# Optimization experiments

Measured on AMD Instinct MI355X. Metric: run time of the kernel, lower is better.

The kernel has to match this reference:

```python
import jax, jax.numpy as jnp
import numpy as np

NEG_SLOPE = 0.2
LN_EPS = 1e-5


def setup_inputs() -> dict:
    key = jax.random.key(0)
    ks = jax.random.split(key, 8)
    N, F, d, L, H = 100000, 128, 64, 3, 4
    dh = d // H
    E = 1600000
    return {
        "x": jax.random.normal(ks[0], (N, F), dtype=jnp.float32),
        "edge_index": jax.random.randint(ks[1], (2, E), 0, N, dtype=jnp.int64),
        "W_enc": jax.random.normal(ks[2], (F, d), dtype=jnp.float32) / np.sqrt(F),
        "b_enc": jnp.zeros((d,), jnp.float32),
        "Wl": jax.random.normal(ks[3], (L, d, d), dtype=jnp.float32) / np.sqrt(d),
        "bl": jnp.zeros((L, d), jnp.float32),
        "Wr": jax.random.normal(ks[4], (L, d, d), dtype=jnp.float32) / np.sqrt(d),
        "br": jnp.zeros((L, d), jnp.float32),
        "att": jax.random.normal(ks[5], (L, H, dh), dtype=jnp.float32) / np.sqrt(dh),
        "out_bias": jnp.zeros((L, d), jnp.float32),
        "gamma": jnp.ones((L, d), jnp.float32),
        "beta": jnp.zeros((L, d), jnp.float32),
    }


def _elu(x):
    return jnp.where(x > 0, x, jnp.expm1(x))


def reference(x, edge_index, W_enc, b_enc, Wl, bl, Wr, br, att, out_bias, gamma, beta):
    N = x.shape[0]
    L, H, dh = att.shape
    d = H * dh
    # PyG GATv2Conv default add_self_loops=True
    loops = jnp.arange(N, dtype=edge_index.dtype)
    src = jnp.concatenate([edge_index[0], loops])  # message source
    dst = jnp.concatenate([edge_index[1], loops])  # aggregation target

    h = jax.nn.relu(x @ W_enc + b_enc)  # [N, d]
    for l in range(L):
        xl = (h @ Wl[l] + bl[l]).reshape(N, H, dh)
        xr = (h @ Wr[l] + br[l]).reshape(N, H, dh)
        # GATv2: score = a^T LeakyReLU(xl[src] + xr[dst])  -> [E, H]
        e = jax.nn.leaky_relu(xl[src] + xr[dst], NEG_SLOPE)
        score = jnp.einsum('ehd,hd->eh', e, att[l])
        # segment softmax over incoming edges of each dst node
        smax = jax.ops.segment_max(score, dst, num_segments=N)
        ex = jnp.exp(score - smax[dst])
        denom = jax.ops.segment_sum(ex, dst, num_segments=N)
        alpha = ex / denom[dst]  # [E, H]
        agg = jax.ops.segment_sum(alpha[:, :, None] * xl[src], dst, num_segments=N)
        hc = agg.reshape(N, d) + out_bias[l]
        # LayerNorm
        mu = hc.mean(-1, keepdims=True)
        var = ((hc - mu) ** 2).mean(-1, keepdims=True)
        hn = (hc - mu) * jax.lax.rsqrt(var + LN_EPS) * gamma[l] + beta[l]
        h = _elu(hn)  # dropout p=0.0 -> identity
    return h
```

## Files before the change

### kernel.cpp

```cpp
#include <hip/hip_runtime.h>
#include <hip/hip_fp16.h>
#include <math.h>

static constexpr int D = 64;
static constexpr int F = 128;
static constexpr int BK = 64;
static constexpr float NEG_SLOPE = 0.2f;
static constexpr float LN_EPS = 1e-5f;
static constexpr float LOG2E = 1.44269504088896340736f;
static constexpr int NCHUNK = 8;

template <int CTRL>
__device__ __forceinline__ float dpp_add(float x) {
  int v = __builtin_amdgcn_update_dpp(0, __float_as_int(x), CTRL, 0xF, 0xF, true);
  return x + __int_as_float(v);
}
__device__ __forceinline__ float red8(float x) {
  x = dpp_add<0xB1>(x);
  x = dpp_add<0x4E>(x);
  x = dpp_add<0x141>(x);
  return x;
}
__device__ __forceinline__ float red16(float x) {
  x = red8(x);
  x = dpp_add<0x140>(x);
  return x;
}
__device__ __forceinline__ float red32(float x) {
  x = red16(x);
  x += __shfl_xor(x, 16);
  return x;
}

__device__ __forceinline__ __half2 h2max(__half2 a, __half2 b) {
  int ai = __builtin_bit_cast(int, a), bi = __builtin_bit_cast(int, b), r;
  asm("v_pk_max_f16 %0, %1, %2" : "=v"(r) : "v"(ai), "v"(bi));
  return __builtin_bit_cast(__half2, r);
}

typedef _Float16 half2_t __attribute__((ext_vector_type(2)));
__device__ __forceinline__ float fdot2f(__half2 a, __half2 b) {
#if __has_builtin(__builtin_amdgcn_fdot2)
  return __builtin_amdgcn_fdot2(__builtin_bit_cast(half2_t, a),
                                __builtin_bit_cast(half2_t, b), 0.f, false);
#else
  float2 af = __half22float2(a), bf = __half22float2(b);
  return fmaf(af.x, bf.x, af.y * bf.y);
#endif
}


__global__ __launch_bounds__(256) void k_scatter(const int* __restrict__ src,
                                                 const int* __restrict__ dst,
                                                 int* __restrict__ cursor,
                                                 int* __restrict__ ssrc, int E, int N) {
  int c = blockIdx.x & (NCHUNK - 1);
  int b0 = (c * N) / NCHUNK, b1 = ((c + 1) * N) / NCHUNK;
  int stride = (gridDim.x / NCHUNK) * 256;
  for (int e = (blockIdx.x >> 3) * 256 + threadIdx.x; e < E; e += stride) {
    int d = dst[e];
    if (d >= b0 && d < b1) {
      int p = atomicAdd(&cursor[d], 1);
      if (p < BK) ssrc[(d << 6) + p] = src[e];
    }
  }
}


__global__ __launch_bounds__(256) void k_encoder(const float* __restrict__ x,
                                                 const float* __restrict__ W,
                                                 const float* __restrict__ b,
                                                 float* __restrict__ h, int N) {
  __shared__ float xT[F][64];
  __shared__ float Ws[F][64];
  int t = threadIdx.x;
  int n0 = blockIdx.x * 64;
  for (int i = t; i < F * D / 4; i += 256)
    ((float4*)&Ws[0][0])[i] = ((const float4*)W)[i];
  {
    int r = t & 63, kq = (t >> 6) * 4;
    int n = n0 + r;
#pragma unroll
    for (int i = 0; i < 8; ++i) {
      int k0 = kq + 16 * i;
      float4 v = (n < N) ? *(const float4*)&x[(size_t)n * F + k0]
                         : make_float4(0.f, 0.f, 0.f, 0.f);
      xT[k0][r] = v.x; xT[k0 + 1][r] = v.y; xT[k0 + 2][r] = v.z; xT[k0 + 3][r] = v.w;
    }
  }
  __syncthreads();
  int c4 = (t & 15) * 4, n4 = (t >> 4) * 4;
  float acc[4][4];
#pragma unroll
  for (int i = 0; i < 4; ++i)
#pragma unroll
    for (int j = 0; j < 4; ++j) acc[i][j] = b[c4 + j];
#pragma unroll 4
  for (int k = 0; k < F; ++k) {
    float4 xv = *(const float4*)&xT[k][n4];
    float4 wv = *(const float4*)&Ws[k][c4];
    const float* xp = (const float*)&xv;
    const float* wp = (const float*)&wv;
#pragma unroll
    for (int i = 0; i < 4; ++i)
#pragma unroll
      for (int j = 0; j < 4; ++j) acc[i][j] = fmaf(xp[i], wp[j], acc[i][j]);
  }
#pragma unroll
  for (int i = 0; i < 4; ++i) {
    int n = n0 + n4 + i;
    if (n < N) {
      float4 o = make_float4(fmaxf(acc[i][0], 0.f), fmaxf(acc[i][1], 0.f),
                             fmaxf(acc[i][2], 0.f), fmaxf(acc[i][3], 0.f));
      *(float4*)&h[(size_t)n * D + c4] = o;
    }
  }
}


__global__ __launch_bounds__(256) void k_layer_gemm(const float* __restrict__ h,
                                                    const float* __restrict__ Wl,
                                                    const float* __restrict__ bl,
                                                    const float* __restrict__ Wr,
                                                    const float* __restrict__ br,
                                                    ushort* __restrict__ xlh,
                                                    float* __restrict__ xr, int N) {
  __shared__ float hT[D][64];
  __shared__ float Wls[D][64];
  __shared__ float Wrs[D][64];
  int t = threadIdx.x;
  int n0 = blockIdx.x * 64;
  for (int i = t; i < D * D / 4; i += 256) {
    ((float4*)&Wls[0][0])[i] = ((const float4*)Wl)[i];
    ((float4*)&Wrs[0][0])[i] = ((const float4*)Wr)[i];
  }
  {
    int r = t & 63, kq = (t >> 6) * 4;
    int n = n0 + r;
#pragma unroll
    for (int i = 0; i < 4; ++i) {
      int k0 = kq + 16 * i;
      float4 v = (n < N) ? *(const float4*)&h[(size_t)n * D + k0]
                         : make_float4(0.f, 0.f, 0.f, 0.f);
      hT[k0][r] = v.x; hT[k0 + 1][r] = v.y; hT[k0 + 2][r] = v.z; hT[k0 + 3][r] = v.w;
    }
  }
  __syncthreads();
  int c4 = (t & 15) * 4, n4 = (t >> 4) * 4;
  float aL[4][4], aR[4][4];
#pragma unroll
  for (int i = 0; i < 4; ++i)
#pragma unroll
    for (int j = 0; j < 4; ++j) { aL[i][j] = bl[c4 + j]; aR[i][j] = br[c4 + j]; }
#pragma unroll 4
  for (int k = 0; k < D; ++k) {
    float4 xv = *(const float4*)&hT[k][n4];
    float4 lv = *(const float4*)&Wls[k][c4];
    float4 rv = *(const float4*)&Wrs[k][c4];
    const float* xp = (const float*)&xv;
    const float* lp = (const float*)&lv;
    const float* rp = (const float*)&rv;
#pragma unroll
    for (int i = 0; i < 4; ++i)
#pragma unroll
      for (int j = 0; j < 4; ++j) {
        aL[i][j] = fmaf(xp[i], lp[j], aL[i][j]);
        aR[i][j] = fmaf(xp[i], rp[j], aR[i][j]);
      }
  }
#pragma unroll
  for (int i = 0; i < 4; ++i) {
    int n = n0 + n4 + i;
    if (n < N) {
      ushort4 o;
      o.x = __half_as_ushort(__float2half_rn(aL[i][0]));
      o.y = __half_as_ushort(__float2half_rn(aL[i][1]));
      o.z = __half_as_ushort(__float2half_rn(aL[i][2]));
      o.w = __half_as_ushort(__float2half_rn(aL[i][3]));
      *(ushort4*)&xlh[(size_t)n * D + c4] = o;
      *(float4*)&xr[(size_t)n * D + c4] =
          make_float4(aR[i][0], aR[i][1], aR[i][2], aR[i][3]);
    }
  }
}


template <int P>
__device__ __forceinline__ void batchH(const char* __restrict__ xlb,
                                       const int* __restrict__ srow,
                                       int slot0, int cnt, int voff, int nd,
                                       __half2 xr2, __half2 a2, __half2 ns2,
                                       float& m, float& s, float& a0, float& a1) {
  int sj[P];
#pragma unroll
  for (int g = 0; g < P / 4; ++g) {
    int4 q = *(const int4*)(srow + slot0 + 4 * g);
    sj[4 * g + 0] = q.x; sj[4 * g + 1] = q.y;
    sj[4 * g + 2] = q.z; sj[4 * g + 3] = q.w;
  }
#pragma unroll
  for (int j = 0; j < P; ++j)
    if (slot0 + j >= cnt) sj[j] = nd;
  __half2 xsv[P];
  float p[P];
#pragma unroll
  for (int j = 0; j < P; ++j)
    xsv[j] = *(const __half2*)(xlb + (((uint32_t)sj[j] << 7) | (uint32_t)voff));
#pragma unroll
  for (int j = 0; j < P; ++j) {
    __half2 v2 = __hadd2(xsv[j], xr2);
    __half2 lr2 = h2max(v2, __hmul2(v2, ns2));
    float pj = red8(fdot2f(a2, lr2));
    p[j] = (slot0 + j < cnt) ? pj : -3.0e38f;
  }
  float pmax = p[0];
#pragma unroll
  for (int j = 1; j < P; ++j) pmax = fmaxf(pmax, p[j]);
  float mnew = fmaxf(m, pmax);
  float c = __builtin_amdgcn_exp2f(m - mnew);
  s *= c; a0 *= c; a1 *= c;
#pragma unroll
  for (int j = 0; j < P; ++j) {
    float w = __builtin_amdgcn_exp2f(p[j] - mnew);
    s += w;
    a0 = fmaf(w, __low2float(xsv[j]), a0);
    a1 = fmaf(w, __high2float(xsv[j]), a1);
  }
  m = mnew;
}

__global__ __launch_bounds__(256) void k_edge_layer(const __half* __restrict__ xlh,
                                                    const float* __restrict__ xr,
                                                    const int* __restrict__ cnt_arr,
                                                    const int* __restrict__ ssrc,
                                                    const float* __restrict__ att_l,
                                                    const float* __restrict__ ob_l,
                                                    const float* __restrict__ g_l,
                                                    const float* __restrict__ be_l,
                                                    float* __restrict__ out, int N) {
  int lane = threadIdx.x & 63;
  int c2 = lane & 31, half = lane >> 5;
  int voff = c2 * 4;
  int wid = threadIdx.x >> 6;
  int wave = blockIdx.x * 4 + wid;
  int nw = gridDim.x * 4;
  const char* xlb = (const char*)xlh;
  float2 af = make_float2(att_l[2 * c2] * LOG2E, att_l[2 * c2 + 1] * LOG2E);
  __half2 a2 = __float22half2_rn(af);
  __half2 ns2 = __float2half2_rn(NEG_SLOPE);
  float2 ob = *(const float2*)&ob_l[2 * c2];
  float2 gm = *(const float2*)&g_l[2 * c2];
  float2 bt = *(const float2*)&be_l[2 * c2];
  int npairs = (N + 1) >> 1;
  for (int ip = wave; ip < npairs; ip += nw) {
    int node = 2 * ip + half;
    bool valid = node < N;
    int nd = valid ? node : N - 1;
    __half2 xr2 = __float22half2_rn(*(const float2*)&xr[(size_t)nd * D + 2 * c2]);
    int cnt = min(cnt_arr[nd], BK);
    const int* srow = ssrc + (nd << 6);
    __half2 xss = *(const __half2*)(xlb + (((uint32_t)nd << 7) | (uint32_t)voff));
    __half2 vs = __hadd2(xss, xr2);
    __half2 ls = h2max(vs, __hmul2(vs, ns2));
    float m = red8(fdot2f(a2, ls));
    float s = 1.f;
    float a0 = __low2float(xss), a1 = __high2float(xss);
    if (cnt > 0)
      batchH<16>(xlb, srow, 0, cnt, voff, nd, xr2, a2, ns2, m, s, a0, a1);
    for (int slot = 16; slot < cnt; slot += 4)
      batchH<4>(xlb, srow, slot, cnt, voff, nd, xr2, a2, ns2, m, s, a0, a1);
    float rs = __builtin_amdgcn_rcpf(s);
    float r0 = fmaf(a0, rs, ob.x);
    float r1 = fmaf(a1, rs, ob.y);
    float mu = red32(r0 + r1) * (1.f / 64.f);
    float d0 = r0 - mu, d1 = r1 - mu;
    float var = red32(fmaf(d0, d0, d1 * d1)) * (1.f / 64.f);
    float rstd = rsqrtf(var + LN_EPS);
    float h0 = fmaf(d0 * rstd, gm.x, bt.x);
    float h1 = fmaf(d1 * rstd, gm.y, bt.y);
    h0 = h0 > 0.f ? h0 : expm1f(h0);
    h1 = h1 > 0.f ? h1 : expm1f(h1);
    if (valid)
      *(float2*)&out[(size_t)node * D + 2 * c2] = make_float2(h0, h1);
  }
}


extern "C" void kernel_launch(void* const* d_in, const int* in_sizes, int n_in,
                              void* d_out, int out_size, void* d_ws, size_t ws_size,
                              hipStream_t stream) {
  const float* x      = (const float*)d_in[0];
  const int*   ei     = (const int*)d_in[1];
  const float* W_enc  = (const float*)d_in[2];
  const float* b_enc  = (const float*)d_in[3];
  const float* Wl     = (const float*)d_in[4];
  const float* bl     = (const float*)d_in[5];
  const float* Wr     = (const float*)d_in[6];
  const float* br     = (const float*)d_in[7];
  const float* att    = (const float*)d_in[8];
  const float* obias  = (const float*)d_in[9];
  const float* gamma  = (const float*)d_in[10];
  const float* beta   = (const float*)d_in[11];

  int N = in_sizes[0] / F;
  int E = in_sizes[1] / 2;
  const int* src = ei;
  const int* dst = ei + E;

  auto align = [](size_t v) { return (v + 255) & ~(size_t)255; };
  char* ws = (char*)d_ws;
  float* h  = (float*)ws;   ws += align((size_t)N * D * 4);
  ushort* xlh = (ushort*)ws; ws += align((size_t)N * D * 2);
  float* xr = (float*)ws;   ws += align((size_t)N * D * 4);
  int* cursor = (int*)ws;   ws += align((size_t)N * 4);
  int* ssrc   = (int*)ws;   ws += align(((size_t)N * BK + 16) * 4);

  int tblk = (N + 63) / 64;

  hipMemsetAsync(cursor, 0, (size_t)N * 4, stream);
  k_scatter<<<2048, 256, 0, stream>>>(src, dst, cursor, ssrc, E, N);

  k_encoder<<<tblk, 256, 0, stream>>>(x, W_enc, b_enc, h, N);

  for (int l = 0; l < 3; ++l) {
    k_layer_gemm<<<tblk, 256, 0, stream>>>(h, Wl + l * D * D, bl + l * D,
                                           Wr + l * D * D, br + l * D, xlh, xr, N);
    float* out = (l == 2) ? (float*)d_out : h;
    k_edge_layer<<<2048, 256, 0, stream>>>((const __half*)xlh, xr, cursor, ssrc,
                                           att + l * 64, obias + l * 64,
                                           gamma + l * 64, beta + l * 64, out, N);
  }
}
```

Before: 368.9 us.

## Process four nodes per wave with 4 channels per lane in edge kernel

The edge aggregation kernel now maps each wave to four destination nodes with 16 lanes per node, each lane handling four channels via 8-byte gathers instead of two nodes with 32 lanes of two channels. Head score reduction shrinks from an 8-lane to a 4-lane DPP reduction, and LayerNorm uses a 16-lane reduction with no cross-half shuffle. This halves the number of gather instructions and the reduction steps per edge, at the cost of more registers per lane and a different load-balance granularity across nodes with uneven degree.

After: 334.3 us. 1.1x faster.

```diff
diff --git a/kernel.cpp b/kernel.cpp
--- a/kernel.cpp
+++ b/kernel.cpp
@@ -15,20 +15,15 @@
   int v = __builtin_amdgcn_update_dpp(0, __float_as_int(x), CTRL, 0xF, 0xF, true);
   return x + __int_as_float(v);
 }
-__device__ __forceinline__ float red8(float x) {
+__device__ __forceinline__ float red4(float x) {
   x = dpp_add<0xB1>(x);
   x = dpp_add<0x4E>(x);
+  return x;
+}
+__device__ __forceinline__ float red16(float x) {
+  x = red4(x);
   x = dpp_add<0x141>(x);
-  return x;
-}
-__device__ __forceinline__ float red16(float x) {
-  x = red8(x);
   x = dpp_add<0x140>(x);
-  return x;
-}
-__device__ __forceinline__ float red32(float x) {
-  x = red16(x);
-  x += __shfl_xor(x, 16);
   return x;
 }
 
@@ -39,13 +34,13 @@
 }
 
 typedef _Float16 half2_t __attribute__((ext_vector_type(2)));
-__device__ __forceinline__ float fdot2f(__half2 a, __half2 b) {
+__device__ __forceinline__ float fdot2f(__half2 a, __half2 b, float c) {
 #if __has_builtin(__builtin_amdgcn_fdot2)
   return __builtin_amdgcn_fdot2(__builtin_bit_cast(half2_t, a),
-                                __builtin_bit_cast(half2_t, b), 0.f, false);
+                                __builtin_bit_cast(half2_t, b), c, false);
 #else
   float2 af = __half22float2(a), bf = __half22float2(b);
-  return fmaf(af.x, bf.x, af.y * bf.y);
+  return fmaf(af.x, bf.x, fmaf(af.y, bf.y, c));
 #endif
 }
 
@@ -185,12 +180,15 @@
 }
 
 
+struct Q4 { float x, y, z, w; };
+
 template <int P>
-__device__ __forceinline__ void batchH(const char* __restrict__ xlb,
+__device__ __forceinline__ void batchQ(const char* __restrict__ xlb,
                                        const int* __restrict__ srow,
                                        int slot0, int cnt, int voff, int nd,
-                                       __half2 xr2, __half2 a2, __half2 ns2,
-                                       float& m, float& s, float& a0, float& a1) {
+                                       __half2 xr_lo, __half2 xr_hi,
+                                       __half2 a_lo, __half2 a_hi, __half2 ns2,
+                                       float& m, float& s, Q4& acc) {
   int sj[P];
 #pragma unroll
   for (int g = 0; g < P / 4; ++g) {
@@ -201,30 +199,37 @@
 #pragma unroll
   for (int j = 0; j < P; ++j)
     if (slot0 + j >= cnt) sj[j] = nd;
-  __half2 xsv[P];
+  uint2 xsv[P];
   float p[P];
 #pragma unroll
   for (int j = 0; j < P; ++j)
-    xsv[j] = *(const __half2*)(xlb + (((uint32_t)sj[j] << 7) | (uint32_t)voff));
+    xsv[j] = *(const uint2*)(xlb + (((uint32_t)sj[j] << 7) | (uint32_t)voff));
 #pragma unroll
   for (int j = 0; j < P; ++j) {
-    __half2 v2 = __hadd2(xsv[j], xr2);
-    __half2 lr2 = h2max(v2, __hmul2(v2, ns2));
-    float pj = red8(fdot2f(a2, lr2));
-    p[j] = (slot0 + j < cnt) ? pj : -3.0e38f;
+    __half2 lo = __builtin_bit_cast(__half2, xsv[j].x);
+    __half2 hi = __builtin_bit_cast(__half2, xsv[j].y);
+    __half2 vlo = __hadd2(lo, xr_lo), vhi = __hadd2(hi, xr_hi);
+    __half2 llo = h2max(vlo, __hmul2(vlo, ns2));
+    __half2 lhi = h2max(vhi, __hmul2(vhi, ns2));
+    float d = red4(fdot2f(a_hi, lhi, fdot2f(a_lo, llo, 0.f)));
+    p[j] = (slot0 + j < cnt) ? d : -3.0e38f;
   }
   float pmax = p[0];
 #pragma unroll
   for (int j = 1; j < P; ++j) pmax = fmaxf(pmax, p[j]);
   float mnew = fmaxf(m, pmax);
   float c = __builtin_amdgcn_exp2f(m - mnew);
-  s *= c; a0 *= c; a1 *= c;
+  s *= c; acc.x *= c; acc.y *= c; acc.z *= c; acc.w *= c;
 #pragma unroll
   for (int j = 0; j < P; ++j) {
     float w = __builtin_amdgcn_exp2f(p[j] - mnew);
     s += w;
-    a0 = fmaf(w, __low2float(xsv[j]), a0);
-    a1 = fmaf(w, __high2float(xsv[j]), a1);
+    __half2 lo = __builtin_bit_cast(__half2, xsv[j].x);
+    __half2 hi = __builtin_bit_cast(__half2, xsv[j].y);
+    acc.x = fmaf(w, __low2float(lo), acc.x);
+    acc.y = fmaf(w, __high2float(lo), acc.y);
+    acc.z = fmaf(w, __low2float(hi), acc.z);
+    acc.w = fmaf(w, __high2float(hi), acc.w);
   }
   m = mnew;
 }
@@ -239,49 +244,61 @@
                                                     const float* __restrict__ be_l,
                                                     float* __restrict__ out, int N) {
   int lane = threadIdx.x & 63;
-  int c2 = lane & 31, half = lane >> 5;
-  int voff = c2 * 4;
+  int c4l = lane & 15, quad = lane >> 4;
+  int voff = c4l * 8;
   int wid = threadIdx.x >> 6;
   int wave = blockIdx.x * 4 + wid;
   int nw = gridDim.x * 4;
   const char* xlb = (const char*)xlh;
-  float2 af = make_float2(att_l[2 * c2] * LOG2E, att_l[2 * c2 + 1] * LOG2E);
-  __half2 a2 = __float22half2_rn(af);
+  float4 af = *(const float4*)&att_l[4 * c4l];
+  __half2 a_lo = __float22half2_rn(make_float2(af.x * LOG2E, af.y * LOG2E));
+  __half2 a_hi = __float22half2_rn(make_float2(af.z * LOG2E, af.w * LOG2E));
   __half2 ns2 = __float2half2_rn(NEG_SLOPE);
-  float2 ob = *(const float2*)&ob_l[2 * c2];
-  float2 gm = *(const float2*)&g_l[2 * c2];
-  float2 bt = *(const float2*)&be_l[2 * c2];
-  int npairs = (N + 1) >> 1;
-  for (int ip = wave; ip < npairs; ip += nw) {
-    int node = 2 * ip + half;
+  float4 ob = *(const float4*)&ob_l[4 * c4l];
+  float4 gm = *(const float4*)&g_l[4 * c4l];
+  float4 bt = *(const float4*)&be_l[4 * c4l];
+  int nquads = (N + 3) >> 2;
+  for (int ip = wave; ip < nquads; ip += nw) {
+    int node = 4 * ip + quad;
     bool valid = node < N;
     int nd = valid ? node : N - 1;
-    __half2 xr2 = __float22half2_rn(*(const float2*)&xr[(size_t)nd * D + 2 * c2]);
+    float4 xrf = *(const float4*)&xr[(size_t)nd * D + 4 * c4l];
+    __half2 xr_lo = __float22half2_rn(make_float2(xrf.x, xrf.y));
+    __half2 xr_hi = __float22half2_rn(make_float2(xrf.z, xrf.w));
     int cnt = min(cnt_arr[nd], BK);
     const int* srow = ssrc + (nd << 6);
-    __half2 xss = *(const __half2*)(xlb + (((uint32_t)nd << 7) | (uint32_t)voff));
-    __half2 vs = __hadd2(xss, xr2);
-    __half2 ls = h2max(vs, __hmul2(vs, ns2));
-    float m = red8(fdot2f(a2, ls));
+    uint2 xss = *(const uint2*)(xlb + (((uint32_t)nd << 7) | (uint32_t)voff));
+    __half2 slo = __builtin_bit_cast(__half2, xss.x);
+    __half2 shi = __builtin_bit_cast(__half2, xss.y);
+    __half2 vlo = __hadd2(slo, xr_lo), vhi = __hadd2(shi, xr_hi);
+    __half2 llo = h2max(vlo, __hmul2(vlo, ns2));
+    __half2 lhi = h2max(vhi, __hmul2(vhi, ns2));
+    float m = red4(fdot2f(a_hi, lhi, fdot2f(a_lo, llo, 0.f)));
     float s = 1.f;
-    float a0 = __low2float(xss), a1 = __high2float(xss);
+    Q4 acc{__low2float(slo), __high2float(slo), __low2float(shi), __high2float(shi)};
     if (cnt > 0)
-      batchH<16>(xlb, srow, 0, cnt, voff, nd, xr2, a2, ns2, m, s, a0, a1);
+      batchQ<16>(xlb, srow, 0, cnt, voff, nd, xr_lo, xr_hi, a_lo, a_hi, ns2, m, s, acc);
     for (int slot = 16; slot < cnt; slot += 4)
-      batchH<4>(xlb, srow, slot, cnt, voff, nd, xr2, a2, ns2, m, s, a0, a1);
+      batchQ<4>(xlb, srow, slot, cnt, voff, nd, xr_lo, xr_hi, a_lo, a_hi, ns2, m, s, acc);
     float rs = __builtin_amdgcn_rcpf(s);
-    float r0 = fmaf(a0, rs, ob.x);
-    float r1 = fmaf(a1, rs, ob.y);
-    float mu = red32(r0 + r1) * (1.f / 64.f);
-    float d0 = r0 - mu, d1 = r1 - mu;
-    float var = red32(fmaf(d0, d0, d1 * d1)) * (1.f / 64.f);
+    float r0 = fmaf(acc.x, rs, ob.x);
+    float r1 = fmaf(acc.y, rs, ob.y);
+    float r2 = fmaf(acc.z, rs, ob.z);
+    float r3 = fmaf(acc.w, rs, ob.w);
+    float mu = red16(r0 + r1 + r2 + r3) * (1.f / 64.f);
+    float d0 = r0 - mu, d1 = r1 - mu, d2 = r2 - mu, d3 = r3 - mu;
+    float var = red16(fmaf(d0, d0, fmaf(d1, d1, fmaf(d2, d2, d3 * d3)))) * (1.f / 64.f);
     float rstd = rsqrtf(var + LN_EPS);
     float h0 = fmaf(d0 * rstd, gm.x, bt.x);
     float h1 = fmaf(d1 * rstd, gm.y, bt.y);
+    float h2 = fmaf(d2 * rstd, gm.z, bt.z);
+    float h3 = fmaf(d3 * rstd, gm.w, bt.w);
     h0 = h0 > 0.f ? h0 : expm1f(h0);
     h1 = h1 > 0.f ? h1 : expm1f(h1);
+    h2 = h2 > 0.f ? h2 : expm1f(h2);
+    h3 = h3 > 0.f ? h3 : expm1f(h3);
     if (valid)
-      *(float2*)&out[(size_t)node * D + 2 * c2] = make_float2(h0, h1);
+      *(float4*)&out[(size_t)node * D + 4 * c4l] = make_float4(h0, h1, h2, h3);
   }
 }
 
```
